# Optimization experiments

Measured on AMD Instinct MI355X. Metric: run time of the kernel, lower is better.

## Reference

```python
import jax, jax.numpy as jnp
import numpy as np

IN_FEATURES = 2048
OUT_FEATURES = 8192
STRIPE_SIZE = 128
NUM_STRIPES = OUT_FEATURES // STRIPE_SIZE


def setup_inputs() -> dict:
    key = jax.random.key(0)
    k_x, k_w, k_t, k_mu, k_std = jax.random.split(key, 5)
    x = jax.random.normal(k_x, (2, 256, IN_FEATURES), dtype=jnp.float32)
    weight = jax.random.normal(k_w, (IN_FEATURES, OUT_FEATURES), dtype=jnp.float32) / np.sqrt(IN_FEATURES)
    bias = jnp.zeros((OUT_FEATURES,), dtype=jnp.float32)
    thresholds = jax.random.uniform(k_t, (NUM_STRIPES, IN_FEATURES), dtype=jnp.float32)
    mu = jax.random.normal(k_mu, (IN_FEATURES,), dtype=jnp.float32)          # adj_med_computed buffer
    std = jax.random.uniform(k_std, (IN_FEATURES,), dtype=jnp.float32)       # adj_std_computed buffer
    return {"x": x, "weight": weight, "bias": bias, "thresholds": thresholds, "mu": mu, "std": std}


def reference(x, weight, bias, thresholds, mu, std):
    # Eval-mode, batch>1 path of CWICLinear.forward.
    og_shape = x.shape[:-1]
    I, O, N, S = IN_FEATURES, OUT_FEATURES, NUM_STRIPES, STRIPE_SIZE
    xc = x.reshape(-1, 1, I) - mu[None, None, :]              # (T, 1, I) centered
    thresh = (thresholds * std[None, :])[None]                # (1, N, I)
    mask = (jnp.abs(xc) > thresh).astype(x.dtype)             # (T, N, I) data-dependent sparsity
    xm = xc * mask                                            # (T, N, I)
    W = weight.T.reshape(N, S, I)                             # stripe view of weight
    y = jnp.einsum('nsi,tni->tns', W, xm).reshape(-1, O)      # stripe matmul
    post_mu = mu @ weight                                     # einsum('a b, a -> b')
    y = y + post_mu[None, :] + bias[None, :]
    flops_const = jnp.float32(I) * jnp.float32(O)
    flops_dense = jnp.zeros(og_shape, dtype=jnp.float32) + flops_const
    flops_sparse = flops_const * mask.mean(-1).mean(-1).reshape(og_shape)
    return (y.reshape(*og_shape, O), flops_dense, flops_sparse)
```

## Files before the change

kernel.cpp:

```cpp
#include <hip/hip_runtime.h>
#include <hip/hip_bf16.h>
#include <stdint.h>

#define I_DIM 2048
#define O_DIM 8192
#define T_TOK 512
#define NSTR  64
#define BK    64
#define NSTEP (I_DIM / BK)

#define TILE_B 16384

#define THR_S 16384
#define SMEM20 24576

#define WT_OFF   ((size_t)0)
#define XC_OFF   ((size_t)67108864)
#define THR_OFF  ((size_t)71303168)
#define PM_OFF   ((size_t)71827456)
#define PMB_OFF  ((size_t)73924608)
#define CNT_OFF  ((size_t)73957376)

typedef __attribute__((ext_vector_type(8))) short bf16x8;
typedef __attribute__((ext_vector_type(4))) float f32x4;
typedef __attribute__((ext_vector_type(4))) int i32x4;

__global__ void cwic_prep(const float* __restrict__ x, const float* __restrict__ mu,
                          const float* __restrict__ thresholds,
                          const float* __restrict__ stdv, float* __restrict__ xc,
                          float* __restrict__ thrs, int* __restrict__ counts) {
  int idx = blockIdx.x * 256 + threadIdx.x;
  float4 xv = ((const float4*)x)[idx];
  float4 mv = ((const float4*)mu)[idx & 511];
  float4 r;
  r.x = xv.x - mv.x; r.y = xv.y - mv.y; r.z = xv.z - mv.z; r.w = xv.w - mv.w;
  ((float4*)xc)[idx] = r;
  if (idx < (NSTR * I_DIM) / 4) {
    float4 t = ((const float4*)thresholds)[idx];
    float4 s = ((const float4*)stdv)[idx & 511];
    float4 ts;
    ts.x = t.x * s.x; ts.y = t.y * s.y; ts.z = t.z * s.z; ts.w = t.w * s.w;
    ((float4*)thrs)[idx] = ts;
  }
  if (idx < T_TOK) counts[idx] = 0;
}

__global__ __launch_bounds__(256) void cwic_wprep2(const float* __restrict__ w,
                                                   const float* __restrict__ mu,
                                                   char* __restrict__ wt,
                                                   float* __restrict__ pm_part) {
  const int bp = blockIdx.x;
  const int hs = bp >> 4;
  const int cc = bp & 15;
  const int step = hs >> 1, kh = hs & 1;
  const int r0 = hs * 32;
  const int tid = threadIdx.x;
  __shared__ float ls[32][512];

  {
    const int sr = tid >> 7, sf = tid & 127;
    #pragma unroll 4
    for (int p = 0; p < 16; ++p) {
      const int row = p * 2 + sr;
      float4 v = *(const float4*)(w + (size_t)(r0 + row) * O_DIM + cc * 512 + sf * 4);
      *(float4*)&ls[row][sf * 4] = v;
    }
  }
  __syncthreads();

  float mus[32];
  #pragma unroll
  for (int r = 0; r < 32; ++r) mus[r] = mu[r0 + r];

  #pragma unroll
  for (int ci = 0; ci < 2; ++ci) {
    const int c = tid + ci * 256;
    const int C = cc * 512 + c;
    const int n = C >> 7, o = C & 127;
    char* tb = wt + (size_t)(n * NSTEP + step) * TILE_B + (kh * 8 + (o >> 4)) * 1024;
    float pm = 0.0f;
    #pragma unroll
    for (int g = 0; g < 4; ++g) {
      unsigned hv[4];
      unsigned hprev = 0;
      #pragma unroll
      for (int e = 0; e < 8; ++e) {
        float v = ls[g * 8 + e][c];
        pm += mus[g * 8 + e] * v;
        unsigned u = __builtin_bit_cast(unsigned, v);
        unsigned r = u + 0x7fffu + ((u >> 16) & 1u);
        unsigned short h = (unsigned short)(r >> 16);
        if ((e & 1) == 0) hprev = h;
        else hv[e >> 1] = hprev | (((unsigned)h) << 16);
      }
      *(i32x4*)(tb + ((o & 15) + g * 16) * 16) = *(i32x4*)hv;
    }
    pm_part[(size_t)(step * 2 + kh) * O_DIM + C] = pm;
  }
}

__global__ void cwic_pmb(const float* __restrict__ pm_part,
                         const float* __restrict__ bias, float* __restrict__ pmb) {
  int o = blockIdx.x * 256 + threadIdx.x;
  float s = bias[o];
  #pragma unroll 8
  for (int j = 0; j < 64; ++j) s += pm_part[(size_t)j * O_DIM + o];
  pmb[o] = s;
}

__global__ __launch_bounds__(512, 4) void cwic_gemm20(
    const float* __restrict__ xc, const char* __restrict__ wt,
    const float* __restrict__ thrs, const float* __restrict__ pmb,
    float* __restrict__ y, int* __restrict__ counts) {
  extern __shared__ char smem[];
  const int b = blockIdx.x;
  const int nid = (b & 7) * 64 + (b >> 3);
  const int n = nid >> 3, tt = nid & 7;
  const int trow0 = tt * 64, ocol0 = n * 128;
  const int tid = threadIdx.x;
  const int lane = tid & 63, wid = tid >> 6;
  const int wr = wid >> 2, wc = wid & 3;
  const int l15 = lane & 15, l4 = lane >> 4;
  const int t_loc = tid >> 3, kq = tid & 7;

  float* thr_s = (float*)(smem + THR_S);
  ((float4*)thr_s)[tid] = ((const float4*)(thrs + (size_t)n * I_DIM))[tid];
  __syncthreads();

  const float* xrow = xc + (size_t)(trow0 + t_loc) * I_DIM + kq * 8;
  const char* wfrag = wt + (size_t)(n * NSTEP) * TILE_B + (wc * 2) * 1024 + lane * 16;

  f32x4 acc[2][2];
  #pragma unroll
  for (int mi = 0; mi < 2; ++mi)
    #pragma unroll
    for (int ni = 0; ni < 2; ++ni) acc[mi][ni] = (f32x4)(0.0f);
  int cnt = 0;

  for (int step = 0; step < NSTEP; ++step) {
    const int abase = (step & 1) * 8192;
    bf16x8 bfr[4];
    {
      const char* bp_ = wfrag + (size_t)step * TILE_B;
      #pragma unroll
      for (int f = 0; f < 4; ++f)
        bfr[f] = *(const bf16x8*)(bp_ + (((f >> 1) * 8) + (f & 1)) * 1024);
    }
    float4 xv0 = *(const float4*)(xrow + step * BK);
    float4 xv1 = *(const float4*)(xrow + step * BK + 4);
    float4 tv0 = *(const float4*)(thr_s + step * BK + kq * 8);
    float4 tv1 = *(const float4*)(thr_s + step * BK + kq * 8 + 4);
    {
      const float xs[8] = {xv0.x, xv0.y, xv0.z, xv0.w, xv1.x, xv1.y, xv1.z, xv1.w};
      const float ts[8] = {tv0.x, tv0.y, tv0.z, tv0.w, tv1.x, tv1.y, tv1.z, tv1.w};
      bf16x8 hv8;
      #pragma unroll
      for (int e = 0; e < 8; ++e) {
        const float xvv = xs[e], tvv = ts[e];
        bool keep = fabsf(xvv) > tvv;
        cnt += keep ? 1 : 0;
        float a = keep ? xvv : 0.0f;
        __hip_bfloat16 h = __float2bfloat16(a);
        hv8[e] = __builtin_bit_cast(short, h);
      }
      const int ad = t_loc * 128 + ((kq * 16) ^ ((t_loc & 7) << 4));
      *(bf16x8*)(smem + abase + ad) = hv8;
    }
    __syncthreads();
    __builtin_amdgcn_s_setprio(1);
    #pragma unroll
    for (int s32 = 0; s32 < 2; ++s32) {
      bf16x8 afh[2];
      #pragma unroll
      for (int mi = 0; mi < 2; ++mi) {
        const int r = wr * 32 + mi * 16 + l15;
        const int ada = r * 128 + (((s32 * 64) + l4 * 16) ^ ((r & 7) << 4));
        afh[mi] = *(const bf16x8*)(smem + abase + ada);
      }
      #pragma unroll
      for (int ni = 0; ni < 2; ++ni) {
        bf16x8 bh = bfr[s32 * 2 + ni];
        #pragma unroll
        for (int mi = 0; mi < 2; ++mi) {
          acc[mi][ni] = __builtin_amdgcn_mfma_f32_16x16x32_bf16(afh[mi], bh, acc[mi][ni], 0, 0, 0);
        }
      }
    }
    __builtin_amdgcn_s_setprio(0);
  }

  cnt += __shfl_xor(cnt, 1);
  cnt += __shfl_xor(cnt, 2);
  cnt += __shfl_xor(cnt, 4);
  if (kq == 0) atomicAdd(&counts[trow0 + t_loc], cnt);

  #pragma unroll
  for (int ni = 0; ni < 2; ++ni) {
    const int o = ocol0 + wc * 32 + ni * 16 + l15;
    const float pv = pmb[o];
    #pragma unroll
    for (int mi = 0; mi < 2; ++mi) {
      const int row0 = trow0 + wr * 32 + mi * 16 + l4 * 4;
      #pragma unroll
      for (int r = 0; r < 4; ++r) {
        y[(size_t)(row0 + r) * O_DIM + o] = acc[mi][ni][r] + pv;
      }
    }
  }
}

__global__ void cwic_fin(const int* __restrict__ counts, float* __restrict__ outF) {
  int t = blockIdx.x * 256 + threadIdx.x;
  outF[t] = 16777216.0f;
  outF[T_TOK + t] = 128.0f * (float)counts[t];
}

extern "C" void kernel_launch(void* const* d_in, const int* in_sizes, int n_in,
                              void* d_out, int out_size, void* d_ws, size_t ws_size,
                              hipStream_t stream) {
  const float* x = (const float*)d_in[0];
  const float* w = (const float*)d_in[1];
  const float* bias = (const float*)d_in[2];
  const float* thresholds = (const float*)d_in[3];
  const float* mu = (const float*)d_in[4];
  const float* stdv = (const float*)d_in[5];
  float* y = (float*)d_out;

  char* ws = (char*)d_ws;
  char* wt = ws + WT_OFF;
  float* xc = (float*)(ws + XC_OFF);
  float* thrs = (float*)(ws + THR_OFF);
  float* pm_part = (float*)(ws + PM_OFF);
  float* pmb = (float*)(ws + PMB_OFF);
  int* counts = (int*)(ws + CNT_OFF);

  cwic_prep<<<1024, 256, 0, stream>>>(x, mu, thresholds, stdv, xc, thrs, counts);
  cwic_wprep2<<<1024, 256, 0, stream>>>(w, mu, wt, pm_part);
  cwic_pmb<<<32, 256, 0, stream>>>(pm_part, bias, pmb);
  cwic_gemm20<<<512, 512, SMEM20, stream>>>(xc, wt, thrs, pmb, y, counts);
  cwic_fin<<<2, 256, 0, stream>>>(counts, y + (size_t)T_TOK * O_DIM);
}
```

Measured before the change: 67.11 us.

## Merge prep kernels and prefetch next-step weight fragments in GEMM

After: 62.43 us. 7.0% less time.

```diff
diff --git a/kernel.cpp b/kernel.cpp
--- a/kernel.cpp
+++ b/kernel.cpp
@@ -12,7 +12,7 @@
 #define TILE_B 16384
 
 #define THR_S 16384
-#define SMEM20 24576
+#define SMEM21 24576
 
 #define WT_OFF   ((size_t)0)
 #define XC_OFF   ((size_t)67108864)
@@ -25,38 +25,37 @@
 typedef __attribute__((ext_vector_type(4))) float f32x4;
 typedef __attribute__((ext_vector_type(4))) int i32x4;
 
-__global__ void cwic_prep(const float* __restrict__ x, const float* __restrict__ mu,
-                          const float* __restrict__ thresholds,
-                          const float* __restrict__ stdv, float* __restrict__ xc,
-                          float* __restrict__ thrs, int* __restrict__ counts) {
-  int idx = blockIdx.x * 256 + threadIdx.x;
-  float4 xv = ((const float4*)x)[idx];
-  float4 mv = ((const float4*)mu)[idx & 511];
-  float4 r;
-  r.x = xv.x - mv.x; r.y = xv.y - mv.y; r.z = xv.z - mv.z; r.w = xv.w - mv.w;
-  ((float4*)xc)[idx] = r;
-  if (idx < (NSTR * I_DIM) / 4) {
-    float4 t = ((const float4*)thresholds)[idx];
-    float4 s = ((const float4*)stdv)[idx & 511];
-    float4 ts;
-    ts.x = t.x * s.x; ts.y = t.y * s.y; ts.z = t.z * s.z; ts.w = t.w * s.w;
-    ((float4*)thrs)[idx] = ts;
-  }
-  if (idx < T_TOK) counts[idx] = 0;
-}
-
-__global__ __launch_bounds__(256) void cwic_wprep2(const float* __restrict__ w,
-                                                   const float* __restrict__ mu,
-                                                   char* __restrict__ wt,
-                                                   float* __restrict__ pm_part) {
+__global__ __launch_bounds__(256) void cwic_prep_all(
+    const float* __restrict__ w, const float* __restrict__ mu,
+    const float* __restrict__ x, const float* __restrict__ thresholds,
+    const float* __restrict__ stdv, char* __restrict__ wt,
+    float* __restrict__ pm_part, float* __restrict__ xc,
+    float* __restrict__ thrs, int* __restrict__ counts) {
+  const int tid = threadIdx.x;
+  __shared__ float ls[32][512];
+
+  if (blockIdx.x >= 1024) {
+    int idx = (blockIdx.x - 1024) * 256 + tid;
+    float4 xv = ((const float4*)x)[idx];
+    float4 mv = ((const float4*)mu)[idx & 511];
+    float4 r;
+    r.x = xv.x - mv.x; r.y = xv.y - mv.y; r.z = xv.z - mv.z; r.w = xv.w - mv.w;
+    ((float4*)xc)[idx] = r;
+    if (idx < (NSTR * I_DIM) / 4) {
+      float4 t = ((const float4*)thresholds)[idx];
+      float4 s = ((const float4*)stdv)[idx & 511];
+      float4 ts;
+      ts.x = t.x * s.x; ts.y = t.y * s.y; ts.z = t.z * s.z; ts.w = t.w * s.w;
+      ((float4*)thrs)[idx] = ts;
+    }
+    if (idx < T_TOK) counts[idx] = 0;
+    return;
+  }
+
   const int bp = blockIdx.x;
-  const int hs = bp >> 4;
-  const int cc = bp & 15;
+  const int hs = bp >> 4, cc = bp & 15;
   const int step = hs >> 1, kh = hs & 1;
   const int r0 = hs * 32;
-  const int tid = threadIdx.x;
-  __shared__ float ls[32][512];
-
   {
     const int sr = tid >> 7, sf = tid & 127;
     #pragma unroll 4
@@ -108,7 +107,7 @@
   pmb[o] = s;
 }
 
-__global__ __launch_bounds__(512, 4) void cwic_gemm20(
+__global__ __launch_bounds__(512, 4) void cwic_gemm21(
     const float* __restrict__ xc, const char* __restrict__ wt,
     const float* __restrict__ thrs, const float* __restrict__ pmb,
     float* __restrict__ y, int* __restrict__ counts) {
@@ -125,7 +124,6 @@
 
   float* thr_s = (float*)(smem + THR_S);
   ((float4*)thr_s)[tid] = ((const float4*)(thrs + (size_t)n * I_DIM))[tid];
-  __syncthreads();
 
   const float* xrow = xc + (size_t)(trow0 + t_loc) * I_DIM + kq * 8;
   const char* wfrag = wt + (size_t)(n * NSTEP) * TILE_B + (wc * 2) * 1024 + lane * 16;
@@ -137,57 +135,71 @@
     for (int ni = 0; ni < 2; ++ni) acc[mi][ni] = (f32x4)(0.0f);
   int cnt = 0;
 
-  for (int step = 0; step < NSTEP; ++step) {
-    const int abase = (step & 1) * 8192;
-    bf16x8 bfr[4];
-    {
-      const char* bp_ = wfrag + (size_t)step * TILE_B;
-      #pragma unroll
-      for (int f = 0; f < 4; ++f)
-        bfr[f] = *(const bf16x8*)(bp_ + (((f >> 1) * 8) + (f & 1)) * 1024);
-    }
-    float4 xv0 = *(const float4*)(xrow + step * BK);
-    float4 xv1 = *(const float4*)(xrow + step * BK + 4);
-    float4 tv0 = *(const float4*)(thr_s + step * BK + kq * 8);
-    float4 tv1 = *(const float4*)(thr_s + step * BK + kq * 8 + 4);
-    {
-      const float xs[8] = {xv0.x, xv0.y, xv0.z, xv0.w, xv1.x, xv1.y, xv1.z, xv1.w};
-      const float ts[8] = {tv0.x, tv0.y, tv0.z, tv0.w, tv1.x, tv1.y, tv1.z, tv1.w};
-      bf16x8 hv8;
-      #pragma unroll
-      for (int e = 0; e < 8; ++e) {
-        const float xvv = xs[e], tvv = ts[e];
-        bool keep = fabsf(xvv) > tvv;
-        cnt += keep ? 1 : 0;
-        float a = keep ? xvv : 0.0f;
-        __hip_bfloat16 h = __float2bfloat16(a);
-        hv8[e] = __builtin_bit_cast(short, h);
-      }
-      const int ad = t_loc * 128 + ((kq * 16) ^ ((t_loc & 7) << 4));
-      *(bf16x8*)(smem + abase + ad) = hv8;
-    }
-    __syncthreads();
-    __builtin_amdgcn_s_setprio(1);
-    #pragma unroll
-    for (int s32 = 0; s32 < 2; ++s32) {
-      bf16x8 afh[2];
-      #pragma unroll
-      for (int mi = 0; mi < 2; ++mi) {
-        const int r = wr * 32 + mi * 16 + l15;
-        const int ada = r * 128 + (((s32 * 64) + l4 * 16) ^ ((r & 7) << 4));
-        afh[mi] = *(const bf16x8*)(smem + abase + ada);
-      }
-      #pragma unroll
-      for (int ni = 0; ni < 2; ++ni) {
-        bf16x8 bh = bfr[s32 * 2 + ni];
-        #pragma unroll
-        for (int mi = 0; mi < 2; ++mi) {
-          acc[mi][ni] = __builtin_amdgcn_mfma_f32_16x16x32_bf16(afh[mi], bh, acc[mi][ni], 0, 0, 0);
-        }
-      }
-    }
-    __builtin_amdgcn_s_setprio(0);
-  }
+  bf16x8 bA0, bA1, bA2, bA3, bB0, bB1, bB2, bB3;
+  bA0 = *(const bf16x8*)(wfrag + 0 * 1024);
+  bA1 = *(const bf16x8*)(wfrag + 1 * 1024);
+  bA2 = *(const bf16x8*)(wfrag + 8 * 1024);
+  bA3 = *(const bf16x8*)(wfrag + 9 * 1024);
+  __syncthreads();
+
+#define STEP21(STEP_I, CUR, B0, B1, B2, B3, NB0, NB1, NB2, NB3)                \
+  {                                                                            \
+    const int step_ = (STEP_I);                                                \
+    const int s1_ = (step_ + 1 < NSTEP) ? step_ + 1 : step_;                   \
+             \
+    {                                                                          \
+      const char* bp_ = wfrag + (size_t)s1_ * TILE_B;                          \
+      NB0 = *(const bf16x8*)(bp_ + 0 * 1024);                                  \
+      NB1 = *(const bf16x8*)(bp_ + 1 * 1024);                                  \
+      NB2 = *(const bf16x8*)(bp_ + 8 * 1024);                                  \
+      NB3 = *(const bf16x8*)(bp_ + 9 * 1024);                                  \
+    }                                                                          \
+        \
+    {                                                                          \
+      float4 xv0 = *(const float4*)(xrow + step_ * BK);                        \
+      float4 xv1 = *(const float4*)(xrow + step_ * BK + 4);                    \
+      float4 tv0 = *(const float4*)(thr_s + step_ * BK + kq * 8);              \
+      float4 tv1 = *(const float4*)(thr_s + step_ * BK + kq * 8 + 4);          \
+      const float xs[8] = {xv0.x, xv0.y, xv0.z, xv0.w, xv1.x, xv1.y, xv1.z, xv1.w}; \
+      const float ts[8] = {tv0.x, tv0.y, tv0.z, tv0.w, tv1.x, tv1.y, tv1.z, tv1.w}; \
+      bf16x8 hv8;                                                              \
+      _Pragma("unroll") for (int e = 0; e < 8; ++e) {                          \
+        const float xvv = xs[e], tvv = ts[e];                                  \
+        bool keep = fabsf(xvv) > tvv;                                          \
+        cnt += keep ? 1 : 0;                                                   \
+        float a = keep ? xvv : 0.0f;                                           \
+        __hip_bfloat16 h = __float2bfloat16(a);                                \
+        hv8[e] = __builtin_bit_cast(short, h);                                 \
+      }                                                                        \
+      const int ad = t_loc * 128 + ((kq * 16) ^ ((t_loc & 7) << 4));           \
+      *(bf16x8*)(smem + (CUR) + ad) = hv8;                                     \
+    }                                                                          \
+    __syncthreads();              \
+               \
+    __builtin_amdgcn_s_setprio(1);                                             \
+    _Pragma("unroll") for (int s32 = 0; s32 < 2; ++s32) {                      \
+      bf16x8 afh[2];                                                           \
+      _Pragma("unroll") for (int mi = 0; mi < 2; ++mi) {                       \
+        const int r = wr * 32 + mi * 16 + l15;                                 \
+        const int ada = r * 128 + (((s32 * 64) + l4 * 16) ^ ((r & 7) << 4));   \
+        afh[mi] = *(const bf16x8*)(smem + (CUR) + ada);                        \
+      }                                                                        \
+      bf16x8 bh0 = (s32 == 0) ? B0 : B2;                                       \
+      bf16x8 bh1 = (s32 == 0) ? B1 : B3;                                       \
+      _Pragma("unroll") for (int mi = 0; mi < 2; ++mi) {                       \
+        acc[mi][0] = __builtin_amdgcn_mfma_f32_16x16x32_bf16(afh[mi], bh0, acc[mi][0], 0, 0, 0); \
+        acc[mi][1] = __builtin_amdgcn_mfma_f32_16x16x32_bf16(afh[mi], bh1, acc[mi][1], 0, 0, 0); \
+      }                                                                        \
+    }                                                                          \
+    __builtin_amdgcn_s_setprio(0);                                             \
+     \
+  }
+
+  for (int sp = 0; sp < NSTEP; sp += 2) {
+    STEP21(sp,     0,    bA0, bA1, bA2, bA3, bB0, bB1, bB2, bB3);
+    STEP21(sp + 1, 8192, bB0, bB1, bB2, bB3, bA0, bA1, bA2, bA3);
+  }
+#undef STEP21
 
   cnt += __shfl_xor(cnt, 1);
   cnt += __shfl_xor(cnt, 2);
@@ -234,9 +246,9 @@
   float* pmb = (float*)(ws + PMB_OFF);
   int* counts = (int*)(ws + CNT_OFF);
 
-  cwic_prep<<<1024, 256, 0, stream>>>(x, mu, thresholds, stdv, xc, thrs, counts);
-  cwic_wprep2<<<1024, 256, 0, stream>>>(w, mu, wt, pm_part);
+  cwic_prep_all<<<2048, 256, 0, stream>>>(w, mu, x, thresholds, stdv, wt,
+                                          pm_part, xc, thrs, counts);
   cwic_pmb<<<32, 256, 0, stream>>>(pm_part, bias, pmb);
-  cwic_gemm20<<<512, 512, SMEM20, stream>>>(xc, wt, thrs, pmb, y, counts);
+  cwic_gemm21<<<512, 512, SMEM21, stream>>>(xc, wt, thrs, pmb, y, counts);
   cwic_fin<<<2, 256, 0, stream>>>(counts, y + (size_t)T_TOK * O_DIM);
 }
```
